# Kernel tuning notes

Measured on AMD Instinct MI355X. Metric: run time of the kernel, lower is better.

Reference implementation:

```python
import jax, jax.numpy as jnp
import numpy as np

NLAYER = 4


def setup_inputs() -> dict:
    key = jax.random.key(0)
    k1, k2, k3 = jax.random.split(key, 3)
    B, T, D, H, L = 32, 512, 512, 512, NLAYER
    scale = 1.0 / np.sqrt(H)
    inputs = jax.random.normal(k1, (B, T, D), dtype=jnp.float32)
    W = jax.random.normal(k2, (L, 3, H, H), dtype=jnp.float32) * scale
    U = jax.random.normal(k3, (L, 3, D, H), dtype=jnp.float32) * scale
    return {"inputs": inputs, "W": W, "U": U}


def _gru_stack(inputs, W, U):
    # inputs: [B, T, D]; W: [L, 3, H, H]; U: [L, 3, D, H]
    L = W.shape[0]
    H = W.shape[-1]
    B = inputs.shape[0]
    x_tbd = jnp.transpose(inputs, (1, 0, 2))  # [T, B, D]
    init = jnp.zeros((L, B, H), dtype=inputs.dtype)

    def step(prev, xt):
        inp = xt
        new_states = []
        for i in range(L):
            z = jax.nn.sigmoid(inp @ U[i, 0] + prev[i] @ W[i, 0])
            r = jax.nn.sigmoid(inp @ U[i, 1] + prev[i] @ W[i, 1])
            h = jnp.tanh(inp @ U[i, 2] + (r * prev[i]) @ W[i, 2])
            s = (1.0 - z) * h + z * prev[i]
            inp = s
            new_states.append(s)
        new = jnp.stack(new_states)  # [L, B, H]
        return new, new_states[-1]  # emit top-layer state

    _, ys = jax.lax.scan(step, init, x_tbd)  # ys: [T, B, H]
    return jnp.transpose(ys, (1, 0, 2))  # [B, T, H]


def reference(inputs, W, U):
    return _gru_stack(inputs, W, U)
```

## Files before the change

kernel.cpp:

```cpp
#include <hip/hip_runtime.h>

#define BB 32
#define TT 512
#define DD 512
#define HH 512
#define LL 4
#define HB (HH * BB)
#define NWG 224
#define TPB 256

#define STATE_FLOATS (LL * 2 * HB)
#define GATE_FLOATS  (3 * LL * HB)
#define DATA_FLOATS  (STATE_FLOATS + GATE_FLOATS)
#define FLAG_STRIDE  64
#define NFLAG        209
#define FLAGS_BYTES  ((unsigned long long)NFLAG * FLAG_STRIDE * 4ull)
#define WS_NEED_BYTES ((unsigned long long)DATA_FLOATS * 4ull + FLAGS_BYTES)

#define KC    64
#define NCH   (HH / KC)
#define IBR   68
#define IBF   (BB * IBR)
#define WLDS  32768
#define LDS_BYTES ((WLDS + 2 * IBF) * 4)

#define DONE_A(f, i) ((f) + (i) * FLAG_STRIDE)
#define DONE_B(f, i) ((f) + (8 + (i)) * FLAG_STRIDE)
#define SPIN_CAP (1 << 22)

__device__ __forceinline__ void wg_wait(int* cnt, int target, int& dead) {
    if (threadIdx.x == 0 && !dead) {
        int spins = 0;
        while (__hip_atomic_load(cnt, __ATOMIC_RELAXED,
                                 __HIP_MEMORY_SCOPE_AGENT) < target) {
            __builtin_amdgcn_s_sleep(2);
            if (++spins > SPIN_CAP) { dead = 1; break; }
        }
        (void)__hip_atomic_load(cnt, __ATOMIC_ACQUIRE,
                                __HIP_MEMORY_SCOPE_AGENT);
    }
    __syncthreads();
}

__device__ __forceinline__ void wg_post(int* cnt) {
    asm volatile("" ::: "memory");
    __builtin_amdgcn_s_waitcnt(0);
    __syncthreads();
    if (threadIdx.x == 0)
        atomicAdd(cnt, 1);
}

__device__ __forceinline__ void pub_store(float* p, float v) {
    __hip_atomic_store(p, v, __ATOMIC_RELAXED, __HIP_MEMORY_SCOPE_AGENT);
}
__device__ __forceinline__ float sigf(float v) {
    return 1.0f / (1.0f + __expf(-v));
}

#define FMA16(WV, E0, E1, E2, E3)                                           \
    acc[0][0] = fmaf(E0, WV.x, acc[0][0]); acc[0][1] = fmaf(E0, WV.y, acc[0][1]); \
    acc[0][2] = fmaf(E0, WV.z, acc[0][2]); acc[0][3] = fmaf(E0, WV.w, acc[0][3]); \
    acc[1][0] = fmaf(E1, WV.x, acc[1][0]); acc[1][1] = fmaf(E1, WV.y, acc[1][1]); \
    acc[1][2] = fmaf(E1, WV.z, acc[1][2]); acc[1][3] = fmaf(E1, WV.w, acc[1][3]); \
    acc[2][0] = fmaf(E2, WV.x, acc[2][0]); acc[2][1] = fmaf(E2, WV.y, acc[2][1]); \
    acc[2][2] = fmaf(E2, WV.z, acc[2][2]); acc[2][3] = fmaf(E2, WV.w, acc[2][3]); \
    acc[3][0] = fmaf(E3, WV.x, acc[3][0]); acc[3][1] = fmaf(E3, WV.y, acc[3][1]); \
    acc[3][2] = fmaf(E3, WV.z, acc[3][2]); acc[3][3] = fmaf(E3, WV.w, acc[3][3])


__global__ __launch_bounds__(TPB) void gru_wave(
    const float* __restrict__ x,
    const float* __restrict__ Wp,
    const float* __restrict__ Up,
    float* __restrict__ out,
    float* __restrict__ ws)
{
    extern __shared__ float lds[];

    const int bid = blockIdx.x;
    const int wg  = (bid & 7) * 28 + (bid >> 3);
    const int tid = threadIdx.x;
    const int sb  = tid >> 4;
    const int sk  = tid & 15;

    float* state = ws;
    float* zbuf  = state + LL * 2 * HB;
    float* rbuf  = zbuf + LL * HB;
    float* hUbuf = rbuf + LL * HB;
    int*   flags = (int*)(ws + DATA_FLOATS);

    float* ib0 = lds + WLDS;
    float* ib1 = ib0 + IBF;

    const bool isZR = wg < 128;
    const bool isHU = (wg >= 128) && (wg < 160);

    int iA = 0, gA = 0, col0 = 0, iB = 0, col0B = 0;
    if (isZR) { int grp = wg >> 4; iA = grp >> 1; gA = grp & 1; col0 = (wg & 15) * 32; }
    else if (isHU) { int w2 = wg - 128; iA = w2 >> 3; col0 = (w2 & 7) * 64; }
    else { int w3 = wg - 160; iB = w3 >> 4; col0B = (w3 & 15) * 32; }

    if (isZR) {
        const float* Um = Up + (size_t)(iA * 3 + gA) * DD * HH + col0;
        const float* Wm = Wp + (size_t)(iA * 3 + gA) * HH * HH + col0;
        for (int u = tid; u < 4096; u += TPB) {
            int k = u >> 3, cc = u & 7;
            *(float4*)&lds[u * 4]         = *(const float4*)&Um[(size_t)k * HH + cc * 4];
            *(float4*)&lds[16384 + u * 4] = *(const float4*)&Wm[(size_t)k * HH + cc * 4];
        }
    } else if (isHU) {
        const float* Mm = Up + (size_t)(iA * 3 + 2) * DD * HH + col0;
        for (int u = tid; u < 8192; u += TPB) {
            int k = u >> 4, cc = u & 15;
            *(float4*)&lds[u * 4] = *(const float4*)&Mm[(size_t)k * HH + cc * 4];
        }
    } else {
        const float* Mm = Wp + (size_t)(iB * 3 + 2) * HH * HH + col0B;
        for (int u = tid; u < 4096; u += TPB) {
            int k = u >> 3, cc = u & 7;
            *(float4*)&lds[u * 4] = *(const float4*)&Mm[(size_t)k * HH + cc * 4];
        }
    }
    __syncthreads();

    int dead = 0;

    if (isZR) {
        const int ksc = tid & 3, cq = (tid >> 2) & 7, bq = tid >> 5;
        const int colq = col0 + cq * 4;
        float* dst = (gA == 0 ? zbuf : rbuf) + (size_t)iA * HB;
        int* cb_up = (iA > 0) ? DONE_B(flags, iA - 1) : nullptr;
        int* cb_my = DONE_B(flags, iA);
        int* c_my  = DONE_A(flags, iA);
        for (int t = 0; t < TT; ++t) {
            float acc[4][4] = {};
            if (cb_up) wg_wait(cb_up, 16 * (t + 1), dead);
            {
                const float* src; size_t rstr;
                if (iA == 0) {
                    src = x + (size_t)sb * TT * DD + (size_t)t * DD + sk * 4;
                    rstr = (size_t)16 * TT * DD;
                } else {
                    src = state + (size_t)((iA - 1) * 2 + (t & 1)) * HB + sb * HH + sk * 4;
                    rstr = (size_t)16 * HH;
                }
                float4 g0 = *(const float4*)&src[0];
                float4 g1 = *(const float4*)&src[rstr];
                src += KC;
                *(float4*)&ib0[sb * IBR + sk * 4]        = g0;
                *(float4*)&ib0[(sb + 16) * IBR + sk * 4] = g1;
                g0 = *(const float4*)&src[0]; g1 = *(const float4*)&src[rstr]; src += KC;
                __syncthreads();
                float *rb = ib0, *nb = ib1;
                const float* wp0 = lds + (ksc * 16 * 8 + cq) * 4;
                for (int c = 0; c < NCH; ++c) {
                    const float* r0 = rb + (bq * 4 + 0) * IBR + ksc * 16;
                    const float* r1 = rb + (bq * 4 + 1) * IBR + ksc * 16;
                    const float* r2 = rb + (bq * 4 + 2) * IBR + ksc * 16;
                    const float* r3 = rb + (bq * 4 + 3) * IBR + ksc * 16;
                    const float* wp = wp0 + c * (KC * 8 * 4);
                    #pragma unroll
                    for (int kk = 0; kk < 4; ++kk) {
                        float4 x0 = *(const float4*)&r0[kk * 4];
                        float4 x1 = *(const float4*)&r1[kk * 4];
                        float4 x2 = *(const float4*)&r2[kk * 4];
                        float4 x3 = *(const float4*)&r3[kk * 4];
                        #pragma unroll
                        for (int j = 0; j < 4; ++j) {
                            float4 wv = *(const float4*)&wp[(kk * 4 + j) * 32];
                            FMA16(wv, (&x0.x)[j], (&x1.x)[j], (&x2.x)[j], (&x3.x)[j]);
                        }
                    }
                    if (c < NCH - 1) {
                        *(float4*)&nb[sb * IBR + sk * 4]        = g0;
                        *(float4*)&nb[(sb + 16) * IBR + sk * 4] = g1;
                        if (c < NCH - 2) {
                            g0 = *(const float4*)&src[0];
                            g1 = *(const float4*)&src[rstr];
                            src += KC;
                        }
                    }
                    __syncthreads();
                    float* tp = rb; rb = nb; nb = tp;
                }
            }
            wg_wait(cb_my, 16 * t, dead);
            {
                const float* src = state + (size_t)(iA * 2 + ((t + 1) & 1)) * HB
                                 + sb * HH + sk * 4;
                const size_t rstr = (size_t)16 * HH;
                float4 g0 = *(const float4*)&src[0];
                float4 g1 = *(const float4*)&src[rstr];
                src += KC;
                *(float4*)&ib0[sb * IBR + sk * 4]        = g0;
                *(float4*)&ib0[(sb + 16) * IBR + sk * 4] = g1;
                g0 = *(const float4*)&src[0]; g1 = *(const float4*)&src[rstr]; src += KC;
                __syncthreads();
                float *rb = ib0, *nb = ib1;
                const float* wp0 = lds + 16384 + (ksc * 16 * 8 + cq) * 4;
                for (int c = 0; c < NCH; ++c) {
                    const float* r0 = rb + (bq * 4 + 0) * IBR + ksc * 16;
                    const float* r1 = rb + (bq * 4 + 1) * IBR + ksc * 16;
                    const float* r2 = rb + (bq * 4 + 2) * IBR + ksc * 16;
                    const float* r3 = rb + (bq * 4 + 3) * IBR + ksc * 16;
                    const float* wp = wp0 + c * (KC * 8 * 4);
                    #pragma unroll
                    for (int kk = 0; kk < 4; ++kk) {
                        float4 x0 = *(const float4*)&r0[kk * 4];
                        float4 x1 = *(const float4*)&r1[kk * 4];
                        float4 x2 = *(const float4*)&r2[kk * 4];
                        float4 x3 = *(const float4*)&r3[kk * 4];
                        #pragma unroll
                        for (int j = 0; j < 4; ++j) {
                            float4 wv = *(const float4*)&wp[(kk * 4 + j) * 32];
                            FMA16(wv, (&x0.x)[j], (&x1.x)[j], (&x2.x)[j], (&x3.x)[j]);
                        }
                    }
                    if (c < NCH - 1) {
                        *(float4*)&nb[sb * IBR + sk * 4]        = g0;
                        *(float4*)&nb[(sb + 16) * IBR + sk * 4] = g1;
                        if (c < NCH - 2) {
                            g0 = *(const float4*)&src[0];
                            g1 = *(const float4*)&src[rstr];
                            src += KC;
                        }
                    }
                    __syncthreads();
                    float* tp = rb; rb = nb; nb = tp;
                }
            }
            #pragma unroll
            for (int i = 0; i < 4; ++i)
                #pragma unroll
                for (int j = 0; j < 4; ++j) {
                    float v = acc[i][j];
                    v += __shfl_xor(v, 1, 64);
                    v += __shfl_xor(v, 2, 64);
                    acc[i][j] = v;
                }
            float s0, s1, s2, s3;
            if      (ksc == 0) { s0 = acc[0][0]; s1 = acc[0][1]; s2 = acc[0][2]; s3 = acc[0][3]; }
            else if (ksc == 1) { s0 = acc[1][0]; s1 = acc[1][1]; s2 = acc[1][2]; s3 = acc[1][3]; }
            else if (ksc == 2) { s0 = acc[2][0]; s1 = acc[2][1]; s2 = acc[2][2]; s3 = acc[2][3]; }
            else               { s0 = acc[3][0]; s1 = acc[3][1]; s2 = acc[3][2]; s3 = acc[3][3]; }
            float* drow = dst + (size_t)(bq * 4 + ksc) * HH + colq;
            pub_store(&drow[0], sigf(s0));
            pub_store(&drow[1], sigf(s1));
            pub_store(&drow[2], sigf(s2));
            pub_store(&drow[3], sigf(s3));
            wg_post(c_my);
        }
    } else if (isHU) {
        const int ks2 = tid & 1, cq = (tid >> 1) & 15, bq = tid >> 5;
        const int colq = col0 + cq * 4;
        float* hu = hUbuf + (size_t)iA * HB;
        int* cb_up = (iA > 0) ? DONE_B(flags, iA - 1) : nullptr;
        int* cb_my = DONE_B(flags, iA);
        int* c_my  = DONE_A(flags, iA);
        for (int t = 0; t < TT; ++t) {
            float acc[4][4] = {};
            if (cb_up) wg_wait(cb_up, 16 * (t + 1), dead);
            {
                const float* src; size_t rstr;
                if (iA == 0) {
                    src = x + (size_t)sb * TT * DD + (size_t)t * DD + sk * 4;
                    rstr = (size_t)16 * TT * DD;
                } else {
                    src = state + (size_t)((iA - 1) * 2 + (t & 1)) * HB + sb * HH + sk * 4;
                    rstr = (size_t)16 * HH;
                }
                float4 g0 = *(const float4*)&src[0];
                float4 g1 = *(const float4*)&src[rstr];
                src += KC;
                *(float4*)&ib0[sb * IBR + sk * 4]        = g0;
                *(float4*)&ib0[(sb + 16) * IBR + sk * 4] = g1;
                g0 = *(const float4*)&src[0]; g1 = *(const float4*)&src[rstr]; src += KC;
                __syncthreads();
                float *rb = ib0, *nb = ib1;
                const float* wp0 = lds + (ks2 * 32 * 16 + cq) * 4;
                for (int c = 0; c < NCH; ++c) {
                    const float* r0 = rb + (bq * 4 + 0) * IBR + ks2 * 32;
                    const float* r1 = rb + (bq * 4 + 1) * IBR + ks2 * 32;
                    const float* r2 = rb + (bq * 4 + 2) * IBR + ks2 * 32;
                    const float* r3 = rb + (bq * 4 + 3) * IBR + ks2 * 32;
                    const float* wp = wp0 + c * (KC * 16 * 4);
                    #pragma unroll
                    for (int kk = 0; kk < 8; ++kk) {
                        float4 x0 = *(const float4*)&r0[kk * 4];
                        float4 x1 = *(const float4*)&r1[kk * 4];
                        float4 x2 = *(const float4*)&r2[kk * 4];
                        float4 x3 = *(const float4*)&r3[kk * 4];
                        #pragma unroll
                        for (int j = 0; j < 4; ++j) {
                            float4 wv = *(const float4*)&wp[(kk * 4 + j) * 64];
                            FMA16(wv, (&x0.x)[j], (&x1.x)[j], (&x2.x)[j], (&x3.x)[j]);
                        }
                    }
                    if (c < NCH - 1) {
                        *(float4*)&nb[sb * IBR + sk * 4]        = g0;
                        *(float4*)&nb[(sb + 16) * IBR + sk * 4] = g1;
                        if (c < NCH - 2) {
                            g0 = *(const float4*)&src[0];
                            g1 = *(const float4*)&src[rstr];
                            src += KC;
                        }
                    }
                    __syncthreads();
                    float* tp = rb; rb = nb; nb = tp;
                }
            }
            wg_wait(cb_my, 16 * t, dead);
            #pragma unroll
            for (int i = 0; i < 4; ++i)
                #pragma unroll
                for (int j = 0; j < 4; ++j) {
                    float v = acc[i][j];
                    v += __shfl_xor(v, 1, 64);
                    acc[i][j] = v;
                }
            float r0v[4], r1v[4];
            if (ks2 == 0) {
                r0v[0]=acc[0][0]; r0v[1]=acc[0][1]; r0v[2]=acc[0][2]; r0v[3]=acc[0][3];
                r1v[0]=acc[1][0]; r1v[1]=acc[1][1]; r1v[2]=acc[1][2]; r1v[3]=acc[1][3];
            } else {
                r0v[0]=acc[2][0]; r0v[1]=acc[2][1]; r0v[2]=acc[2][2]; r0v[3]=acc[2][3];
                r1v[0]=acc[3][0]; r1v[1]=acc[3][1]; r1v[2]=acc[3][2]; r1v[3]=acc[3][3];
            }
            const int b0 = bq * 4 + ks2 * 2;
            float* h0 = hu + (size_t)b0 * HH + colq;
            float* h1 = hu + (size_t)(b0 + 1) * HH + colq;
            pub_store(&h0[0], r0v[0]); pub_store(&h0[1], r0v[1]);
            pub_store(&h0[2], r0v[2]); pub_store(&h0[3], r0v[3]);
            pub_store(&h1[0], r1v[0]); pub_store(&h1[1], r1v[1]);
            pub_store(&h1[2], r1v[2]); pub_store(&h1[3], r1v[3]);
            wg_post(c_my);
        }
    } else {
        const int ksc = tid & 3, cq = (tid >> 2) & 7, bq = tid >> 5;
        const int colq = col0B + cq * 4;
        const float* rbase = rbuf + (size_t)iB * HB;
        const float* hu    = hUbuf + (size_t)iB * HB;
        const float* zz    = zbuf + (size_t)iB * HB;
        int* c_my = DONE_B(flags, iB);
        for (int t = 0; t < TT; ++t) {
            wg_wait(DONE_A(flags, iB), 40 * (t + 1), dead);
            const float* prow = state + (size_t)(iB * 2 + ((t + 1) & 1)) * HB;
            float acc[4][4] = {};
            {
                const float* rs = rbase + (size_t)sb * HH + sk * 4;
                const float* ps = prow  + (size_t)sb * HH + sk * 4;
                const size_t rstr = (size_t)16 * HH;
                float4 g0r = *(const float4*)&rs[0],   g0p = *(const float4*)&ps[0];
                float4 g1r = *(const float4*)&rs[rstr], g1p = *(const float4*)&ps[rstr];
                rs += KC; ps += KC;
                *(float4*)&ib0[sb * IBR + sk * 4] =
                    make_float4(g0r.x * g0p.x, g0r.y * g0p.y, g0r.z * g0p.z, g0r.w * g0p.w);
                *(float4*)&ib0[(sb + 16) * IBR + sk * 4] =
                    make_float4(g1r.x * g1p.x, g1r.y * g1p.y, g1r.z * g1p.z, g1r.w * g1p.w);
                g0r = *(const float4*)&rs[0];   g0p = *(const float4*)&ps[0];
                g1r = *(const float4*)&rs[rstr]; g1p = *(const float4*)&ps[rstr];
                rs += KC; ps += KC;
                __syncthreads();
                float *rb = ib0, *nb = ib1;
                const float* wp0 = lds + (ksc * 16 * 8 + cq) * 4;
                for (int c = 0; c < NCH; ++c) {
                    const float* r0 = rb + (bq * 4 + 0) * IBR + ksc * 16;
                    const float* r1 = rb + (bq * 4 + 1) * IBR + ksc * 16;
                    const float* r2 = rb + (bq * 4 + 2) * IBR + ksc * 16;
                    const float* r3 = rb + (bq * 4 + 3) * IBR + ksc * 16;
                    const float* wp = wp0 + c * (KC * 8 * 4);
                    #pragma unroll
                    for (int kk = 0; kk < 4; ++kk) {
                        float4 x0 = *(const float4*)&r0[kk * 4];
                        float4 x1 = *(const float4*)&r1[kk * 4];
                        float4 x2 = *(const float4*)&r2[kk * 4];
                        float4 x3 = *(const float4*)&r3[kk * 4];
                        #pragma unroll
                        for (int j = 0; j < 4; ++j) {
                            float4 wv = *(const float4*)&wp[(kk * 4 + j) * 32];
                            FMA16(wv, (&x0.x)[j], (&x1.x)[j], (&x2.x)[j], (&x3.x)[j]);
                        }
                    }
                    if (c < NCH - 1) {
                        *(float4*)&nb[sb * IBR + sk * 4] =
                            make_float4(g0r.x * g0p.x, g0r.y * g0p.y, g0r.z * g0p.z, g0r.w * g0p.w);
                        *(float4*)&nb[(sb + 16) * IBR + sk * 4] =
                            make_float4(g1r.x * g1p.x, g1r.y * g1p.y, g1r.z * g1p.z, g1r.w * g1p.w);
                        if (c < NCH - 2) {
                            g0r = *(const float4*)&rs[0];   g0p = *(const float4*)&ps[0];
                            g1r = *(const float4*)&rs[rstr]; g1p = *(const float4*)&ps[rstr];
                            rs += KC; ps += KC;
                        }
                    }
                    __syncthreads();
                    float* tp = rb; rb = nb; nb = tp;
                }
            }
            if (iB < 3) wg_wait(DONE_A(flags, iB + 1), 40 * t, dead);
            #pragma unroll
            for (int i = 0; i < 4; ++i)
                #pragma unroll
                for (int j = 0; j < 4; ++j) {
                    float v = acc[i][j];
                    v += __shfl_xor(v, 1, 64);
                    v += __shfl_xor(v, 2, 64);
                    acc[i][j] = v;
                }
            float s0, s1, s2, s3;
            if      (ksc == 0) { s0 = acc[0][0]; s1 = acc[0][1]; s2 = acc[0][2]; s3 = acc[0][3]; }
            else if (ksc == 1) { s0 = acc[1][0]; s1 = acc[1][1]; s2 = acc[1][2]; s3 = acc[1][3]; }
            else if (ksc == 2) { s0 = acc[2][0]; s1 = acc[2][1]; s2 = acc[2][2]; s3 = acc[2][3]; }
            else               { s0 = acc[3][0]; s1 = acc[3][1]; s2 = acc[3][2]; s3 = acc[3][3]; }
            float* stNew = state + (size_t)(iB * 2 + (t & 1)) * HB;
            const int b = bq * 4 + ksc;
            float4 hu4 = *(const float4*)&hu[(size_t)b * HH + colq];
            float4 zz4 = *(const float4*)&zz[(size_t)b * HH + colq];
            float4 pv4 = *(const float4*)&prow[(size_t)b * HH + colq];
            float av[4] = {s0, s1, s2, s3};
            float4 o4;
            #pragma unroll
            for (int j = 0; j < 4; ++j) {
                float h  = tanhf(av[j] + (&hu4.x)[j]);
                float zg = (&zz4.x)[j];
                float s  = zg * ((&pv4.x)[j] - h) + h;
                pub_store(&stNew[(size_t)b * HH + colq + j], s);
                (&o4.x)[j] = s;
            }
            if (iB == LL - 1)
                *(float4*)&out[((size_t)b * TT + t) * HH + colq] = o4;
            wg_post(c_my);
        }
    }
}

extern "C" void kernel_launch(void* const* d_in, const int* in_sizes, int n_in,
                              void* d_out, int out_size, void* d_ws, size_t ws_size,
                              hipStream_t stream) {
    const float* x  = (const float*)d_in[0];
    const float* Wp = (const float*)d_in[1];
    const float* Up = (const float*)d_in[2];
    float* out = (float*)d_out;
    float* ws  = (float*)d_ws;

    if (ws_size < WS_NEED_BYTES) {
        hipMemsetAsync(d_out, 0x7e, (size_t)out_size * sizeof(float), stream);
        return;
    }

    hipMemsetAsync(ws, 0, (size_t)STATE_FLOATS * sizeof(float), stream);
    hipMemsetAsync(ws + DATA_FLOATS, 0, FLAGS_BYTES, stream);

    hipLaunchKernelGGL(gru_wave, dim3(NWG), dim3(TPB), LDS_BYTES, stream,
                       x, Wp, Up, out, ws);
    hipError_t err = hipGetLastError();
    if (err != hipSuccess)
        hipMemsetAsync(d_out, 0x7f, (size_t)out_size * sizeof(float), stream);
}
```

Baseline: 12.34 ms.

## Shard completion counters four ways and rebalance HU work across 256 workgroups

Each per-layer completion counter becomes four sharded counters, so producer workgroups spread their atomic increments and consumers poll all four in parallel with four lanes. The goal is less atomic contention and lower barrier latency on the per-timestep grid-wide handshakes. The HU gate is also re-split from 32 workgroups with 64 columns to 64 workgroups with 32 columns, so the grid grows to 256 workgroups and the HU tiles match the ZR tiling. The risk is that more co-resident workgroups and more flag polling could add memory traffic, and the kernel relies on all 256 workgroups being resident at once.

```diff
diff --git a/kernel.cpp b/kernel.cpp
--- a/kernel.cpp
+++ b/kernel.cpp
@@ -6,7 +6,7 @@
 #define HH 512
 #define LL 4
 #define HB (HH * BB)
-#define NWG 224
+#define NWG 256
 #define TPB 256
 
 #define STATE_FLOATS (LL * 2 * HB)
@@ -24,30 +24,32 @@
 #define WLDS  32768
 #define LDS_BYTES ((WLDS + 2 * IBF) * 4)
 
-#define DONE_A(f, i) ((f) + (i) * FLAG_STRIDE)
-#define DONE_B(f, i) ((f) + (8 + (i)) * FLAG_STRIDE)
+#define DONE_A(f, i) ((f) + (size_t)(i) * 4 * FLAG_STRIDE)
+#define DONE_B(f, i) ((f) + (size_t)(16 + (i) * 4) * FLAG_STRIDE)
 #define SPIN_CAP (1 << 22)
 
-__device__ __forceinline__ void wg_wait(int* cnt, int target, int& dead) {
-    if (threadIdx.x == 0 && !dead) {
+__device__ __forceinline__ void wait4(volatile int* sdead, int* base, int tgt) {
+    if (threadIdx.x < 4) {
+        int* c = base + threadIdx.x * FLAG_STRIDE;
         int spins = 0;
-        while (__hip_atomic_load(cnt, __ATOMIC_RELAXED,
-                                 __HIP_MEMORY_SCOPE_AGENT) < target) {
+        while (*sdead == 0 &&
+               __hip_atomic_load(c, __ATOMIC_RELAXED,
+                                 __HIP_MEMORY_SCOPE_AGENT) < tgt) {
             __builtin_amdgcn_s_sleep(2);
-            if (++spins > SPIN_CAP) { dead = 1; break; }
-        }
-        (void)__hip_atomic_load(cnt, __ATOMIC_ACQUIRE,
-                                __HIP_MEMORY_SCOPE_AGENT);
+            if (++spins > SPIN_CAP) { *sdead = 1; break; }
+        }
     }
+    if (threadIdx.x == 0)
+        __builtin_amdgcn_fence(__ATOMIC_ACQUIRE, "agent");
     __syncthreads();
 }
 
-__device__ __forceinline__ void wg_post(int* cnt) {
+__device__ __forceinline__ void wg_post(int* shard_cnt) {
     asm volatile("" ::: "memory");
     __builtin_amdgcn_s_waitcnt(0);
     __syncthreads();
     if (threadIdx.x == 0)
-        atomicAdd(cnt, 1);
+        atomicAdd(shard_cnt, 1);
 }
 
 __device__ __forceinline__ void pub_store(float* p, float v) {
@@ -76,12 +78,14 @@
     float* __restrict__ ws)
 {
     extern __shared__ float lds[];
+    __shared__ int s_dead;
 
     const int bid = blockIdx.x;
-    const int wg  = (bid & 7) * 28 + (bid >> 3);
+    const int wg  = (bid & 7) * 32 + (bid >> 3);
     const int tid = threadIdx.x;
     const int sb  = tid >> 4;
     const int sk  = tid & 15;
+    const int shard = wg & 3;
 
     float* state = ws;
     float* zbuf  = state + LL * 2 * HB;
@@ -93,12 +97,12 @@
     float* ib1 = ib0 + IBF;
 
     const bool isZR = wg < 128;
-    const bool isHU = (wg >= 128) && (wg < 160);
+    const bool isHU = (wg >= 128) && (wg < 192);
 
     int iA = 0, gA = 0, col0 = 0, iB = 0, col0B = 0;
     if (isZR) { int grp = wg >> 4; iA = grp >> 1; gA = grp & 1; col0 = (wg & 15) * 32; }
-    else if (isHU) { int w2 = wg - 128; iA = w2 >> 3; col0 = (w2 & 7) * 64; }
-    else { int w3 = wg - 160; iB = w3 >> 4; col0B = (w3 & 15) * 32; }
+    else if (isHU) { int w2 = wg - 128; iA = w2 >> 4; col0 = (w2 & 15) * 32; }
+    else { int w3 = wg - 192; iB = w3 >> 4; col0B = (w3 & 15) * 32; }
 
     if (isZR) {
         const float* Um = Up + (size_t)(iA * 3 + gA) * DD * HH + col0;
@@ -108,33 +112,26 @@
             *(float4*)&lds[u * 4]         = *(const float4*)&Um[(size_t)k * HH + cc * 4];
             *(float4*)&lds[16384 + u * 4] = *(const float4*)&Wm[(size_t)k * HH + cc * 4];
         }
-    } else if (isHU) {
-        const float* Mm = Up + (size_t)(iA * 3 + 2) * DD * HH + col0;
-        for (int u = tid; u < 8192; u += TPB) {
-            int k = u >> 4, cc = u & 15;
-            *(float4*)&lds[u * 4] = *(const float4*)&Mm[(size_t)k * HH + cc * 4];
-        }
     } else {
-        const float* Mm = Wp + (size_t)(iB * 3 + 2) * HH * HH + col0B;
+        const float* Mm = isHU ? (Up + (size_t)(iA * 3 + 2) * DD * HH + col0)
+                               : (Wp + (size_t)(iB * 3 + 2) * HH * HH + col0B);
         for (int u = tid; u < 4096; u += TPB) {
             int k = u >> 3, cc = u & 7;
             *(float4*)&lds[u * 4] = *(const float4*)&Mm[(size_t)k * HH + cc * 4];
         }
     }
+    if (tid == 0) s_dead = 0;
     __syncthreads();
 
-    int dead = 0;
+    const int ksc = tid & 3, cq = (tid >> 2) & 7, bq = tid >> 5;
 
     if (isZR) {
-        const int ksc = tid & 3, cq = (tid >> 2) & 7, bq = tid >> 5;
         const int colq = col0 + cq * 4;
         float* dst = (gA == 0 ? zbuf : rbuf) + (size_t)iA * HB;
-        int* cb_up = (iA > 0) ? DONE_B(flags, iA - 1) : nullptr;
-        int* cb_my = DONE_B(flags, iA);
-        int* c_my  = DONE_A(flags, iA);
+        int* c_my = DONE_A(flags, iA) + shard * FLAG_STRIDE;
         for (int t = 0; t < TT; ++t) {
             float acc[4][4] = {};
-            if (cb_up) wg_wait(cb_up, 16 * (t + 1), dead);
+            if (iA > 0) wait4(&s_dead, DONE_B(flags, iA - 1), 4 * (t + 1));
             {
                 const float* src; size_t rstr;
                 if (iA == 0) {
@@ -184,7 +181,7 @@
                     float* tp = rb; rb = nb; nb = tp;
                 }
             }
-            wg_wait(cb_my, 16 * t, dead);
+            wait4(&s_dead, DONE_B(flags, iA), 4 * t);
             {
                 const float* src = state + (size_t)(iA * 2 + ((t + 1) & 1)) * HB
                                  + sb * HH + sk * 4;
@@ -251,15 +248,12 @@
             wg_post(c_my);
         }
     } else if (isHU) {
-        const int ks2 = tid & 1, cq = (tid >> 1) & 15, bq = tid >> 5;
         const int colq = col0 + cq * 4;
         float* hu = hUbuf + (size_t)iA * HB;
-        int* cb_up = (iA > 0) ? DONE_B(flags, iA - 1) : nullptr;
-        int* cb_my = DONE_B(flags, iA);
-        int* c_my  = DONE_A(flags, iA);
+        int* c_my = DONE_A(flags, iA) + shard * FLAG_STRIDE;
         for (int t = 0; t < TT; ++t) {
             float acc[4][4] = {};
-            if (cb_up) wg_wait(cb_up, 16 * (t + 1), dead);
+            if (iA > 0) wait4(&s_dead, DONE_B(flags, iA - 1), 4 * (t + 1));
             {
                 const float* src; size_t rstr;
                 if (iA == 0) {
@@ -277,22 +271,22 @@
                 g0 = *(const float4*)&src[0]; g1 = *(const float4*)&src[rstr]; src += KC;
                 __syncthreads();
                 float *rb = ib0, *nb = ib1;
-                const float* wp0 = lds + (ks2 * 32 * 16 + cq) * 4;
+                const float* wp0 = lds + (ksc * 16 * 8 + cq) * 4;
                 for (int c = 0; c < NCH; ++c) {
-                    const float* r0 = rb + (bq * 4 + 0) * IBR + ks2 * 32;
-                    const float* r1 = rb + (bq * 4 + 1) * IBR + ks2 * 32;
-                    const float* r2 = rb + (bq * 4 + 2) * IBR + ks2 * 32;
-                    const float* r3 = rb + (bq * 4 + 3) * IBR + ks2 * 32;
-                    const float* wp = wp0 + c * (KC * 16 * 4);
+                    const float* r0 = rb + (bq * 4 + 0) * IBR + ksc * 16;
+                    const float* r1 = rb + (bq * 4 + 1) * IBR + ksc * 16;
+                    const float* r2 = rb + (bq * 4 + 2) * IBR + ksc * 16;
+                    const float* r3 = rb + (bq * 4 + 3) * IBR + ksc * 16;
+                    const float* wp = wp0 + c * (KC * 8 * 4);
                     #pragma unroll
-                    for (int kk = 0; kk < 8; ++kk) {
+                    for (int kk = 0; kk < 4; ++kk) {
                         float4 x0 = *(const float4*)&r0[kk * 4];
                         float4 x1 = *(const float4*)&r1[kk * 4];
                         float4 x2 = *(const float4*)&r2[kk * 4];
                         float4 x3 = *(const float4*)&r3[kk * 4];
                         #pragma unroll
                         for (int j = 0; j < 4; ++j) {
-                            float4 wv = *(const float4*)&wp[(kk * 4 + j) * 64];
+                            float4 wv = *(const float4*)&wp[(kk * 4 + j) * 32];
                             FMA16(wv, (&x0.x)[j], (&x1.x)[j], (&x2.x)[j], (&x3.x)[j]);
                         }
                     }
@@ -309,41 +303,36 @@
                     float* tp = rb; rb = nb; nb = tp;
                 }
             }
-            wg_wait(cb_my, 16 * t, dead);
+            wait4(&s_dead, DONE_B(flags, iA), 4 * t);
             #pragma unroll
             for (int i = 0; i < 4; ++i)
                 #pragma unroll
                 for (int j = 0; j < 4; ++j) {
                     float v = acc[i][j];
                     v += __shfl_xor(v, 1, 64);
+                    v += __shfl_xor(v, 2, 64);
                     acc[i][j] = v;
                 }
-            float r0v[4], r1v[4];
-            if (ks2 == 0) {
-                r0v[0]=acc[0][0]; r0v[1]=acc[0][1]; r0v[2]=acc[0][2]; r0v[3]=acc[0][3];
-                r1v[0]=acc[1][0]; r1v[1]=acc[1][1]; r1v[2]=acc[1][2]; r1v[3]=acc[1][3];
-            } else {
-                r0v[0]=acc[2][0]; r0v[1]=acc[2][1]; r0v[2]=acc[2][2]; r0v[3]=acc[2][3];
-                r1v[0]=acc[3][0]; r1v[1]=acc[3][1]; r1v[2]=acc[3][2]; r1v[3]=acc[3][3];
-            }
-            const int b0 = bq * 4 + ks2 * 2;
-            float* h0 = hu + (size_t)b0 * HH + colq;
-            float* h1 = hu + (size_t)(b0 + 1) * HH + colq;
-            pub_store(&h0[0], r0v[0]); pub_store(&h0[1], r0v[1]);
-            pub_store(&h0[2], r0v[2]); pub_store(&h0[3], r0v[3]);
-            pub_store(&h1[0], r1v[0]); pub_store(&h1[1], r1v[1]);
-            pub_store(&h1[2], r1v[2]); pub_store(&h1[3], r1v[3]);
+            float s0, s1, s2, s3;
+            if      (ksc == 0) { s0 = acc[0][0]; s1 = acc[0][1]; s2 = acc[0][2]; s3 = acc[0][3]; }
+            else if (ksc == 1) { s0 = acc[1][0]; s1 = acc[1][1]; s2 = acc[1][2]; s3 = acc[1][3]; }
+            else if (ksc == 2) { s0 = acc[2][0]; s1 = acc[2][1]; s2 = acc[2][2]; s3 = acc[2][3]; }
+            else               { s0 = acc[3][0]; s1 = acc[3][1]; s2 = acc[3][2]; s3 = acc[3][3]; }
+            float* drow = hu + (size_t)(bq * 4 + ksc) * HH + colq;
+            pub_store(&drow[0], s0);
+            pub_store(&drow[1], s1);
+            pub_store(&drow[2], s2);
+            pub_store(&drow[3], s3);
             wg_post(c_my);
         }
     } else {
-        const int ksc = tid & 3, cq = (tid >> 2) & 7, bq = tid >> 5;
         const int colq = col0B + cq * 4;
         const float* rbase = rbuf + (size_t)iB * HB;
         const float* hu    = hUbuf + (size_t)iB * HB;
         const float* zz    = zbuf + (size_t)iB * HB;
-        int* c_my = DONE_B(flags, iB);
+        int* c_my = DONE_B(flags, iB) + shard * FLAG_STRIDE;
         for (int t = 0; t < TT; ++t) {
-            wg_wait(DONE_A(flags, iB), 40 * (t + 1), dead);
+            wait4(&s_dead, DONE_A(flags, iB), 12 * (t + 1));
             const float* prow = state + (size_t)(iB * 2 + ((t + 1) & 1)) * HB;
             float acc[4][4] = {};
             {
@@ -396,7 +385,7 @@
                     float* tp = rb; rb = nb; nb = tp;
                 }
             }
-            if (iB < 3) wg_wait(DONE_A(flags, iB + 1), 40 * t, dead);
+            if (iB < 3) wait4(&s_dead, DONE_A(flags, iB + 1), 12 * t);
             #pragma unroll
             for (int i = 0; i < 4; ++i)
                 #pragma unroll
```

Measured after the change: 37.07 ms. 200% more time.
